# Optimization experiments

Hardware: AMD Instinct MI355X
Metric: run time of the kernel (lower is better)

## Reference

```python
import jax, jax.numpy as jnp
import numpy as np

NEG = -100000.0

def setup_inputs() -> dict:
    key = jax.random.key(0)
    k1, k2 = jax.random.split(key)
    B, La, Lb, D = 64, 512, 512, 768
    a = jax.random.normal(k1, (B, La, D), dtype=jnp.float32)
    b = jax.random.normal(k2, (B, Lb, D), dtype=jnp.float32)
    mask_a = jnp.ones((B, La), dtype=jnp.int32)
    mask_b = jnp.ones((B, Lb), dtype=jnp.int32)
    return {"a": a, "mask_a": mask_a, "b": b, "mask_b": mask_b}

def reference(a, mask_a, b, mask_b):
    # e: [B, La, Lb] raw alignment scores
    e = jnp.einsum('bid,bjd->bij', a, b)
    # outer-product mask [B, La, Lb]; masked_fill where mask_e < 0.5
    mask_e = mask_a[:, :, None].astype(jnp.float32) * mask_b[:, None, :].astype(jnp.float32)
    e = jnp.where(mask_e < 0.5, NEG, e)
    # softmax over Lb -> attend b for each position of a
    t_a = jnp.einsum('bij,bjd->bid', jax.nn.softmax(e, axis=2), b)
    # softmax over La -> attend a for each position of b (transpose of attn)
    t_b = jnp.einsum('bij,bid->bjd', jax.nn.softmax(e, axis=1), a)
    m_a = jnp.concatenate((a, t_a, a - t_a, a * t_a), axis=-1)
    m_b = jnp.concatenate((b, t_b, b - t_b, b * t_b), axis=-1)
    return (m_a, m_b)
```

## Files before the change

kernel.cpp:

```cpp
#include <hip/hip_runtime.h>
#include <stdint.h>

#define B_  64
#define LA  512
#define LB  512
#define DD  768
#define NEGV -100000.0f

typedef __attribute__((ext_vector_type(8))) short bf16x8;
typedef __attribute__((ext_vector_type(4))) float f32x4;

__device__ __forceinline__ unsigned short f2bf(float x) {
    union { float f; unsigned u; } v; v.f = x;
    unsigned r = v.u + 0x7fffu + ((v.u >> 16) & 1u);
    return (unsigned short)(r >> 16);
}
__device__ __forceinline__ float bf2f(unsigned short h) {
    union { float f; unsigned u; } v; v.u = ((unsigned)h) << 16;
    return v.f;
}

#define GLD16(gp, lp) __builtin_amdgcn_global_load_lds( \
    (const __attribute__((address_space(1))) void*)(gp), \
    (__attribute__((address_space(3))) void*)(lp), 16, 0, 0)

template<int L>
__global__ void prep_k(const float* __restrict__ x,
                       unsigned short* __restrict__ xT,
                       unsigned short* __restrict__ xh,
                       unsigned short* __restrict__ xl) {
    __shared__ unsigned short tile[64][65];
    const int l0 = blockIdx.x * 64, d0 = blockIdx.y * 64, b = blockIdx.z;
    const float* xp = x + (size_t)b * L * DD;
    unsigned short* tp = xT + (size_t)b * DD * L;
    unsigned short* hp = xh + (size_t)b * L * DD;
    unsigned short* lp = xl + (size_t)b * L * DD;
    const int c4 = (threadIdx.x & 15) * 4;
    const int r0 = threadIdx.x >> 4;
#pragma unroll
    for (int s = 0; s < 4; ++s) {
        const int r = r0 + s * 16;
        const int l = l0 + r;
        float4 v = *(const float4*)(xp + (size_t)l * DD + d0 + c4);
        ushort4 h, lo;
        h.x = f2bf(v.x); lo.x = f2bf(v.x - bf2f(h.x));
        h.y = f2bf(v.y); lo.y = f2bf(v.y - bf2f(h.y));
        h.z = f2bf(v.z); lo.z = f2bf(v.z - bf2f(h.z));
        h.w = f2bf(v.w); lo.w = f2bf(v.w - bf2f(h.w));
        tile[r][c4 + 0] = h.x; tile[r][c4 + 1] = h.y;
        tile[r][c4 + 2] = h.z; tile[r][c4 + 3] = h.w;
        const int qp = (((c4 >> 3) ^ (r >> 1)) & 3) << 3;
        const int dp = d0 + (c4 & ~31) + qp + (c4 & 7);
        *(ushort4*)&hp[(size_t)l * DD + dp] = h;
        *(ushort4*)&lp[(size_t)l * DD + dp] = lo;
    }
    __syncthreads();
    const int c = threadIdx.x & 63, rr = threadIdx.x >> 6;
#pragma unroll
    for (int s = 0; s < 16; ++s) {
        const int r = rr + s * 4;
        const int qp = (((c >> 3) ^ (r >> 1)) & 3) << 3;
        const int cp = l0 + (c & ~31) + qp + (c & 7);
        tp[(size_t)(d0 + r) * L + cp] = tile[c][r];
    }
}

__global__ __launch_bounds__(256, 2)
void egemm_k(const unsigned short* __restrict__ Ahg, const unsigned short* __restrict__ Alg,
             const unsigned short* __restrict__ Bhg, const unsigned short* __restrict__ Blg,
             const int* __restrict__ mask_a, const int* __restrict__ mask_b,
             float* __restrict__ e) {
    __shared__ unsigned short Ah[128 * 32], Al[128 * 32], Bh[128 * 32], Bl[128 * 32];
    const int loc = blockIdx.x, g = blockIdx.y;
    const int t = loc >> 3;
    const int bb = g * 8 + (loc & 7);
    const int m0 = (t & 3) * 128, n0 = (t >> 2) * 128;

    const int tid = threadIdx.x;
    const int lane = tid & 63, w = tid >> 6;
    const int wm = (w >> 1) * 64, wn = (w & 1) * 64;
    const int lrow = lane & 15, qsel = lane >> 4;
    const int poff = ((qsel ^ (lrow >> 1)) & 3) << 3;

    const size_t boff = (size_t)bb * 512 * DD;
    const int sr0 = (2 * w) * 16 + (lane >> 2);
    const int sc = (lane & 3) * 8;
    const unsigned short* pa0 = Ahg + boff + (size_t)(m0 + sr0) * DD + sc;
    const unsigned short* pa1 = pa0 + 16 * DD;
    const unsigned short* pl0 = Alg + boff + (size_t)(m0 + sr0) * DD + sc;
    const unsigned short* pl1 = pl0 + 16 * DD;
    const unsigned short* pb0 = Bhg + boff + (size_t)(n0 + sr0) * DD + sc;
    const unsigned short* pb1 = pb0 + 16 * DD;
    const unsigned short* pm0 = Blg + boff + (size_t)(n0 + sr0) * DD + sc;
    const unsigned short* pm1 = pm0 + 16 * DD;
    unsigned short* la0 = &Ah[(2 * w) * 512]; unsigned short* la1 = la0 + 512;
    unsigned short* ll0 = &Al[(2 * w) * 512]; unsigned short* ll1 = ll0 + 512;
    unsigned short* lb0 = &Bh[(2 * w) * 512]; unsigned short* lb1 = lb0 + 512;
    unsigned short* lm0 = &Bl[(2 * w) * 512]; unsigned short* lm1 = lm0 + 512;

    f32x4 acc[4][4] = {};

    for (int k0 = 0; k0 < DD; k0 += 32) {
        GLD16(pa0 + k0, la0); GLD16(pa1 + k0, la1);
        GLD16(pl0 + k0, ll0); GLD16(pl1 + k0, ll1);
        GLD16(pb0 + k0, lb0); GLD16(pb1 + k0, lb1);
        GLD16(pm0 + k0, lm0); GLD16(pm1 + k0, lm1);
        __syncthreads();
        bf16x8 ahf[4], alf[4], bhf[4], blf[4];
#pragma unroll
        for (int mi = 0; mi < 4; ++mi) {
            const int R = wm + mi * 16 + lrow;
            ahf[mi] = *(const bf16x8*)&Ah[R * 32 + poff];
            alf[mi] = *(const bf16x8*)&Al[R * 32 + poff];
        }
#pragma unroll
        for (int ni = 0; ni < 4; ++ni) {
            const int R = wn + ni * 16 + lrow;
            bhf[ni] = *(const bf16x8*)&Bh[R * 32 + poff];
            blf[ni] = *(const bf16x8*)&Bl[R * 32 + poff];
        }
#pragma unroll
        for (int mi = 0; mi < 4; ++mi)
#pragma unroll
            for (int ni = 0; ni < 4; ++ni) {
                acc[mi][ni] = __builtin_amdgcn_mfma_f32_16x16x32_bf16(alf[mi], bhf[ni], acc[mi][ni], 0, 0, 0);
                acc[mi][ni] = __builtin_amdgcn_mfma_f32_16x16x32_bf16(ahf[mi], blf[ni], acc[mi][ni], 0, 0, 0);
                acc[mi][ni] = __builtin_amdgcn_mfma_f32_16x16x32_bf16(ahf[mi], bhf[ni], acc[mi][ni], 0, 0, 0);
            }
        __syncthreads();
    }

    const int* map = mask_a + bb * LA;
    const int* mbp = mask_b + bb * LB;
    float* ep = e + (size_t)bb * LA * LB;
    const int colbase = n0 + wn + (lane & 15);
    const int rowbase = m0 + wm + (lane >> 4) * 4;
#pragma unroll
    for (int mi = 0; mi < 4; ++mi)
#pragma unroll
        for (int ni = 0; ni < 4; ++ni) {
            const int j = colbase + ni * 16;
            const float mbf = (float)mbp[j];
#pragma unroll
            for (int r = 0; r < 4; ++r) {
                const int i = rowbase + mi * 16 + r;
                const float mm = (float)map[i] * mbf;
                const float v = (mm < 0.5f) ? NEGV : acc[mi][ni][r];
                __builtin_nontemporal_store(v, &ep[(size_t)i * LB + j]);
            }
        }
}

__global__ void rowstats_k(const float* __restrict__ e,
                           float* __restrict__ rmax, float* __restrict__ rinv) {
    const int row = blockIdx.x * 4 + (threadIdx.x >> 6);
    const int lane = threadIdx.x & 63;
    const float* ep = e + (size_t)row * LB;
    float4 v1 = *(const float4*)(ep + lane * 8);
    float4 v2 = *(const float4*)(ep + lane * 8 + 4);
    float m = fmaxf(fmaxf(fmaxf(v1.x, v1.y), fmaxf(v1.z, v1.w)),
                    fmaxf(fmaxf(v2.x, v2.y), fmaxf(v2.z, v2.w)));
#pragma unroll
    for (int o = 32; o; o >>= 1) m = fmaxf(m, __shfl_xor(m, o));
    float s = __expf(v1.x - m) + __expf(v1.y - m) + __expf(v1.z - m) + __expf(v1.w - m)
            + __expf(v2.x - m) + __expf(v2.y - m) + __expf(v2.z - m) + __expf(v2.w - m);
#pragma unroll
    for (int o = 32; o; o >>= 1) s += __shfl_xor(s, o);
    if (lane == 0) { rmax[row] = m; rinv[row] = 1.0f / s; }
}

__global__ void colstats_k(const float* __restrict__ e,
                           float* __restrict__ cmax, float* __restrict__ cinv) {
    __shared__ float sm[4][64], ss[4][64];
    const int j0 = blockIdx.x * 64;
    const int bb = blockIdx.y;
    const int jj = threadIdx.x & 63, seg = threadIdx.x >> 6;
    const float* ep = e + (size_t)bb * LA * LB + (size_t)seg * 128 * LB + j0 + jj;
    float m = -3.4e38f, s = 0.f;
    for (int i = 0; i < 128; ++i) {
        const float v = ep[(size_t)i * LB];
        const float nm = fmaxf(m, v);
        s = s * __expf(m - nm) + __expf(v - nm);
        m = nm;
    }
    sm[seg][jj] = m; ss[seg][jj] = s;
    __syncthreads();
    if (seg == 0) {
        const float m0 = sm[0][jj], m1 = sm[1][jj], m2 = sm[2][jj], m3 = sm[3][jj];
        const float M = fmaxf(fmaxf(m0, m1), fmaxf(m2, m3));
        const float S = ss[0][jj] * __expf(m0 - M) + ss[1][jj] * __expf(m1 - M)
                      + ss[2][jj] * __expf(m2 - M) + ss[3][jj] * __expf(m3 - M);
        cmax[bb * LB + j0 + jj] = M;
        cinv[bb * LB + j0 + jj] = 1.0f / S;
    }
}

__global__ void pgen_k(const float* __restrict__ e,
                       const float* __restrict__ rmax, const float* __restrict__ rinv,
                       const float* __restrict__ cmax, const float* __restrict__ cinv,
                       unsigned short* __restrict__ Pa, unsigned short* __restrict__ PbT) {
    __shared__ unsigned short tile[64][65];
    const int i0 = blockIdx.x * 64, j0 = blockIdx.y * 64, bb = blockIdx.z;
    const float* ep = e + (size_t)bb * LA * LB;
    const int c = threadIdx.x & 63, r0 = threadIdx.x >> 6;
    const float cm = cmax[bb * LB + j0 + c];
    const float ci = cinv[bb * LB + j0 + c];
#pragma unroll
    for (int s = 0; s < 16; ++s) {
        const int r = r0 + s * 4;
        const float rm = rmax[bb * LA + i0 + r];
        const float ri = rinv[bb * LA + i0 + r];
        const float v = ep[(size_t)(i0 + r) * LB + j0 + c];
        const int qp = (((c >> 3) ^ (r >> 1)) & 3) << 3;
        const int jp = j0 + (c & ~31) + qp + (c & 7);
        Pa[((size_t)bb * LA + i0 + r) * LB + jp] = f2bf(__expf(v - rm) * ri);
        tile[r][c] = f2bf(__expf(v - cm) * ci);
    }
    __syncthreads();
#pragma unroll
    for (int s = 0; s < 16; ++s) {
        const int r = r0 + s * 4;
        const int qp = (((c >> 3) ^ (r >> 1)) & 3) << 3;
        const int ip = i0 + (c & ~31) + qp + (c & 7);
        PbT[((size_t)bb * LB + j0 + r) * LA + ip] = tile[c][r];
    }
}

__global__ __launch_bounds__(256, 2)
void pv_gemm_k(const unsigned short* __restrict__ P,
               const unsigned short* __restrict__ VT,
               const float* __restrict__ X,
               float* __restrict__ out) {
    constexpr int K = 512;
    __shared__ unsigned short At[128 * 32], Bt[128 * 32];
    const int loc = blockIdx.x, g = blockIdx.y;
    const int t = loc >> 3;
    const int bb = g * 8 + (loc & 7);
    const int m0 = (t & 3) * 128, n0 = (t >> 2) * 128;

    const int tid = threadIdx.x;
    const int lane = tid & 63, w = tid >> 6;
    const int wm = (w >> 1) * 64, wn = (w & 1) * 64;
    const int lrow = lane & 15, qsel = lane >> 4;
    const int poff = ((qsel ^ (lrow >> 1)) & 3) << 3;

    const unsigned short* Pp = P + (size_t)bb * 512 * K;
    const unsigned short* Vp = VT + (size_t)bb * DD * K;
    const int sr0 = (2 * w) * 16 + (lane >> 2);
    const int sc = (lane & 3) * 8;
    const unsigned short* p0 = Pp + (size_t)(m0 + sr0) * K + sc;
    const unsigned short* p1 = p0 + 16 * K;
    const unsigned short* v0 = Vp + (size_t)(n0 + sr0) * K + sc;
    const unsigned short* v1 = v0 + 16 * K;
    unsigned short* lA0 = &At[(2 * w) * 512]; unsigned short* lA1 = lA0 + 512;
    unsigned short* lB0 = &Bt[(2 * w) * 512]; unsigned short* lB1 = lB0 + 512;

    f32x4 acc[4][4] = {};
    for (int k0 = 0; k0 < K; k0 += 32) {
        GLD16(p0 + k0, lA0); GLD16(p1 + k0, lA1);
        GLD16(v0 + k0, lB0); GLD16(v1 + k0, lB1);
        __syncthreads();
        bf16x8 af[4], bf_[4];
#pragma unroll
        for (int mi = 0; mi < 4; ++mi)
            af[mi] = *(const bf16x8*)&At[(wm + mi * 16 + lrow) * 32 + poff];
#pragma unroll
        for (int ni = 0; ni < 4; ++ni)
            bf_[ni] = *(const bf16x8*)&Bt[(wn + ni * 16 + lrow) * 32 + poff];
#pragma unroll
        for (int mi = 0; mi < 4; ++mi)
#pragma unroll
            for (int ni = 0; ni < 4; ++ni)
                acc[mi][ni] = __builtin_amdgcn_mfma_f32_16x16x32_bf16(af[mi], bf_[ni], acc[mi][ni], 0, 0, 0);
        __syncthreads();
    }

    const float* Xp = X + (size_t)bb * 512 * DD;
    float* op = out + (size_t)bb * 512 * (4 * DD);
    const int colbase = n0 + wn + (lane & 15);
    const int rowbase = m0 + wm + (lane >> 4) * 4;
#pragma unroll
    for (int mi = 0; mi < 4; ++mi)
#pragma unroll
        for (int ni = 0; ni < 4; ++ni) {
            const int d = colbase + ni * 16;
#pragma unroll
            for (int r = 0; r < 4; ++r) {
                const int i = rowbase + mi * 16 + r;
                const float tv = acc[mi][ni][r];
                const float xv = Xp[(size_t)i * DD + d];
                float* o = op + (size_t)i * (4 * DD) + d;
                __builtin_nontemporal_store(xv, o);
                __builtin_nontemporal_store(tv, o + DD);
                __builtin_nontemporal_store(xv - tv, o + 2 * DD);
                __builtin_nontemporal_store(xv * tv, o + 3 * DD);
            }
        }
}

extern "C" void kernel_launch(void* const* d_in, const int* in_sizes, int n_in,
                              void* d_out, int out_size, void* d_ws, size_t ws_size,
                              hipStream_t stream) {
    const float* a      = (const float*)d_in[0];
    const int*   mask_a = (const int*)d_in[1];
    const float* b      = (const float*)d_in[2];
    const int*   mask_b = (const int*)d_in[3];
    float* out = (float*)d_out;

    uint8_t* w = (uint8_t*)d_ws;
    float* e            = (float*)w;          w += (size_t)B_ * LA * LB * 4;
    unsigned short* aT  = (unsigned short*)w; w += (size_t)B_ * DD * LA * 2;
    unsigned short* bT  = (unsigned short*)w; w += (size_t)B_ * DD * LB * 2;
    unsigned short* ahi = (unsigned short*)w; w += (size_t)B_ * LA * DD * 2;
    unsigned short* alo = (unsigned short*)w; w += (size_t)B_ * LA * DD * 2;
    unsigned short* bhi = (unsigned short*)w; w += (size_t)B_ * LB * DD * 2;
    unsigned short* blo = (unsigned short*)w; w += (size_t)B_ * LB * DD * 2;
    float* rmax = (float*)w; w += (size_t)B_ * LA * 4;
    float* rinv = (float*)w; w += (size_t)B_ * LA * 4;
    float* cmax = (float*)w; w += (size_t)B_ * LB * 4;
    float* cinv = (float*)w; w += (size_t)B_ * LB * 4;
    unsigned short* Pa  = ahi;
    unsigned short* PbT = ahi + (size_t)B_ * LA * LB;

    prep_k<LA><<<dim3(LA / 64, DD / 64, B_), 256, 0, stream>>>(a, aT, ahi, alo);
    prep_k<LB><<<dim3(LB / 64, DD / 64, B_), 256, 0, stream>>>(b, bT, bhi, blo);
    egemm_k<<<dim3(128, 8), 256, 0, stream>>>(ahi, alo, bhi, blo, mask_a, mask_b, e);
    rowstats_k<<<B_ * LA / 4, 256, 0, stream>>>(e, rmax, rinv);
    colstats_k<<<dim3(LB / 64, B_), 256, 0, stream>>>(e, cmax, cinv);
    pgen_k<<<dim3(LA / 64, LB / 64, B_), 256, 0, stream>>>(e, rmax, rinv, cmax, cinv, Pa, PbT);
    float* out_mb = out + (size_t)B_ * LA * (4 * DD);
    pv_gemm_k<<<dim3(192, 8), 256, 0, stream>>>(Pa, bT, a, out);
    pv_gemm_k<<<dim3(192, 8), 256, 0, stream>>>(PbT, aT, b, out_mb);
}
```

Baseline: 1.362 ms.

## Fuse all stages into one persistent kernel with software grid barriers

Replaces the eight separate launches (prep, score GEMM, row/col stats, probability generation, two PV GEMMs) with one persistent kernel of 512 blocks that loops over work items per phase and synchronises phases with an atomic grid barrier. This removes launch gaps and tail effects between stages and lets the two PV GEMMs share one work pool. Pa/PbT get dedicated workspace instead of aliasing ahi, and the nontemporal store on e is dropped. It risks deadlock if all 512 blocks are not co-resident, and the barriers serialise phases with fixed grid-wide parallelism, which may underuse the GPU in some phases.

```diff
diff --git a/kernel.cpp b/kernel.cpp
--- a/kernel.cpp
+++ b/kernel.cpp
@@ -6,6 +6,7 @@
 #define LB  512
 #define DD  768
 #define NEGV -100000.0f
+#define NB  512
 
 typedef __attribute__((ext_vector_type(8))) short bf16x8;
 typedef __attribute__((ext_vector_type(4))) float f32x4;
@@ -24,278 +25,314 @@
     (const __attribute__((address_space(1))) void*)(gp), \
     (__attribute__((address_space(3))) void*)(lp), 16, 0, 0)
 
-template<int L>
-__global__ void prep_k(const float* __restrict__ x,
-                       unsigned short* __restrict__ xT,
-                       unsigned short* __restrict__ xh,
-                       unsigned short* __restrict__ xl) {
-    __shared__ unsigned short tile[64][65];
-    const int l0 = blockIdx.x * 64, d0 = blockIdx.y * 64, b = blockIdx.z;
-    const float* xp = x + (size_t)b * L * DD;
-    unsigned short* tp = xT + (size_t)b * DD * L;
-    unsigned short* hp = xh + (size_t)b * L * DD;
-    unsigned short* lp = xl + (size_t)b * L * DD;
-    const int c4 = (threadIdx.x & 15) * 4;
-    const int r0 = threadIdx.x >> 4;
-#pragma unroll
-    for (int s = 0; s < 4; ++s) {
-        const int r = r0 + s * 16;
-        const int l = l0 + r;
-        float4 v = *(const float4*)(xp + (size_t)l * DD + d0 + c4);
-        ushort4 h, lo;
-        h.x = f2bf(v.x); lo.x = f2bf(v.x - bf2f(h.x));
-        h.y = f2bf(v.y); lo.y = f2bf(v.y - bf2f(h.y));
-        h.z = f2bf(v.z); lo.z = f2bf(v.z - bf2f(h.z));
-        h.w = f2bf(v.w); lo.w = f2bf(v.w - bf2f(h.w));
-        tile[r][c4 + 0] = h.x; tile[r][c4 + 1] = h.y;
-        tile[r][c4 + 2] = h.z; tile[r][c4 + 3] = h.w;
-        const int qp = (((c4 >> 3) ^ (r >> 1)) & 3) << 3;
-        const int dp = d0 + (c4 & ~31) + qp + (c4 & 7);
-        *(ushort4*)&hp[(size_t)l * DD + dp] = h;
-        *(ushort4*)&lp[(size_t)l * DD + dp] = lo;
-    }
+__device__ __forceinline__ void gridbar(unsigned* cnt, unsigned* gen) {
     __syncthreads();
-    const int c = threadIdx.x & 63, rr = threadIdx.x >> 6;
-#pragma unroll
-    for (int s = 0; s < 16; ++s) {
-        const int r = rr + s * 4;
-        const int qp = (((c >> 3) ^ (r >> 1)) & 3) << 3;
-        const int cp = l0 + (c & ~31) + qp + (c & 7);
-        tp[(size_t)(d0 + r) * L + cp] = tile[c][r];
-    }
+    if (threadIdx.x == 0) {
+        __threadfence();
+        unsigned g0 = __hip_atomic_load(gen, __ATOMIC_ACQUIRE, __HIP_MEMORY_SCOPE_AGENT);
+        unsigned t = __hip_atomic_fetch_add(cnt, 1u, __ATOMIC_ACQ_REL, __HIP_MEMORY_SCOPE_AGENT);
+        if (t == NB - 1) {
+            __hip_atomic_store(cnt, 0u, __ATOMIC_RELAXED, __HIP_MEMORY_SCOPE_AGENT);
+            __hip_atomic_fetch_add(gen, 1u, __ATOMIC_ACQ_REL, __HIP_MEMORY_SCOPE_AGENT);
+        } else {
+            while (__hip_atomic_load(gen, __ATOMIC_ACQUIRE, __HIP_MEMORY_SCOPE_AGENT) == g0)
+                __builtin_amdgcn_s_sleep(8);
+        }
+        __threadfence();
+    }
+    __syncthreads();
+}
+
+__global__ void init_sync_k(unsigned* cnt, unsigned* gen) {
+    if (threadIdx.x == 0) { *cnt = 0u; *gen = 0u; }
 }
 
 __global__ __launch_bounds__(256, 2)
-void egemm_k(const unsigned short* __restrict__ Ahg, const unsigned short* __restrict__ Alg,
-             const unsigned short* __restrict__ Bhg, const unsigned short* __restrict__ Blg,
-             const int* __restrict__ mask_a, const int* __restrict__ mask_b,
-             float* __restrict__ e) {
-    __shared__ unsigned short Ah[128 * 32], Al[128 * 32], Bh[128 * 32], Bl[128 * 32];
-    const int loc = blockIdx.x, g = blockIdx.y;
-    const int t = loc >> 3;
-    const int bb = g * 8 + (loc & 7);
-    const int m0 = (t & 3) * 128, n0 = (t >> 2) * 128;
-
+void mega_k(const float* __restrict__ a, const float* __restrict__ b,
+            const int* __restrict__ mask_a, const int* __restrict__ mask_b,
+            float* __restrict__ e,
+            unsigned short* __restrict__ aT, unsigned short* __restrict__ bT,
+            unsigned short* __restrict__ ahi, unsigned short* __restrict__ alo,
+            unsigned short* __restrict__ bhi, unsigned short* __restrict__ blo,
+            float* __restrict__ rmax, float* __restrict__ rinv,
+            float* __restrict__ cmax, float* __restrict__ cinv,
+            unsigned short* __restrict__ Pa, unsigned short* __restrict__ PbT,
+            float* __restrict__ out_a, float* __restrict__ out_b,
+            unsigned* cnt, unsigned* gen)
+{
+    __shared__ __align__(16) unsigned char SMEM[32768];
+    const int bid = blockIdx.x;
     const int tid = threadIdx.x;
-    const int lane = tid & 63, w = tid >> 6;
-    const int wm = (w >> 1) * 64, wn = (w & 1) * 64;
-    const int lrow = lane & 15, qsel = lane >> 4;
-    const int poff = ((qsel ^ (lrow >> 1)) & 3) << 3;
-
-    const size_t boff = (size_t)bb * 512 * DD;
-    const int sr0 = (2 * w) * 16 + (lane >> 2);
-    const int sc = (lane & 3) * 8;
-    const unsigned short* pa0 = Ahg + boff + (size_t)(m0 + sr0) * DD + sc;
-    const unsigned short* pa1 = pa0 + 16 * DD;
-    const unsigned short* pl0 = Alg + boff + (size_t)(m0 + sr0) * DD + sc;
-    const unsigned short* pl1 = pl0 + 16 * DD;
-    const unsigned short* pb0 = Bhg + boff + (size_t)(n0 + sr0) * DD + sc;
-    const unsigned short* pb1 = pb0 + 16 * DD;
-    const unsigned short* pm0 = Blg + boff + (size_t)(n0 + sr0) * DD + sc;
-    const unsigned short* pm1 = pm0 + 16 * DD;
-    unsigned short* la0 = &Ah[(2 * w) * 512]; unsigned short* la1 = la0 + 512;
-    unsigned short* ll0 = &Al[(2 * w) * 512]; unsigned short* ll1 = ll0 + 512;
-    unsigned short* lb0 = &Bh[(2 * w) * 512]; unsigned short* lb1 = lb0 + 512;
-    unsigned short* lm0 = &Bl[(2 * w) * 512]; unsigned short* lm1 = lm0 + 512;
-
-    f32x4 acc[4][4] = {};
-
-    for (int k0 = 0; k0 < DD; k0 += 32) {
-        GLD16(pa0 + k0, la0); GLD16(pa1 + k0, la1);
-        GLD16(pl0 + k0, ll0); GLD16(pl1 + k0, ll1);
-        GLD16(pb0 + k0, lb0); GLD16(pb1 + k0, lb1);
-        GLD16(pm0 + k0, lm0); GLD16(pm1 + k0, lm1);
+
+    {
+        unsigned short (*tile)[65] = reinterpret_cast<unsigned short(*)[65]>(SMEM);
+        const int c4 = (tid & 15) * 4;
+        const int r0 = tid >> 4;
+        const int c = tid & 63, rr = tid >> 6;
+        for (int job = bid; job < 12288; job += NB) {
+            __syncthreads();
+            const int side = (job >= 6144);
+            const int j = side ? job - 6144 : job;
+            const int x = j & 7, y = (j >> 3) % 12, bb = j / 96;
+            const int l0 = x * 64, d0 = y * 64;
+            const float* xp = (side ? b : a) + (size_t)bb * 512 * DD;
+            unsigned short* tp = (side ? bT : aT) + (size_t)bb * DD * 512;
+            unsigned short* hp = (side ? bhi : ahi) + (size_t)bb * 512 * DD;
+            unsigned short* lp = (side ? blo : alo) + (size_t)bb * 512 * DD;
+#pragma unroll
+            for (int s = 0; s < 4; ++s) {
+                const int r = r0 + s * 16;
+                const int l = l0 + r;
+                float4 v = *(const float4*)(xp + (size_t)l * DD + d0 + c4);
+                ushort4 h, lo;
+                h.x = f2bf(v.x); lo.x = f2bf(v.x - bf2f(h.x));
+                h.y = f2bf(v.y); lo.y = f2bf(v.y - bf2f(h.y));
+                h.z = f2bf(v.z); lo.z = f2bf(v.z - bf2f(h.z));
+                h.w = f2bf(v.w); lo.w = f2bf(v.w - bf2f(h.w));
+                tile[r][c4 + 0] = h.x; tile[r][c4 + 1] = h.y;
+                tile[r][c4 + 2] = h.z; tile[r][c4 + 3] = h.w;
+                const int qp = (((c4 >> 3) ^ (r >> 1)) & 3) << 3;
+                const int dp = d0 + (c4 & ~31) + qp + (c4 & 7);
+                *(ushort4*)&hp[(size_t)l * DD + dp] = h;
+                *(ushort4*)&lp[(size_t)l * DD + dp] = lo;
+            }
+            __syncthreads();
+#pragma unroll
+            for (int s = 0; s < 16; ++s) {
+                const int r = rr + s * 4;
+                const int qp = (((c >> 3) ^ (r >> 1)) & 3) << 3;
+                const int cp = l0 + (c & ~31) + qp + (c & 7);
+                tp[(size_t)(d0 + r) * 512 + cp] = tile[c][r];
+            }
+        }
+    }
+    gridbar(cnt, gen);
+
+    {
+        unsigned short* Ah = (unsigned short*)SMEM;
+        unsigned short* Al = Ah + 4096;
+        unsigned short* Bh = Ah + 8192;
+        unsigned short* Bl = Ah + 12288;
+        const int lane = tid & 63, w = tid >> 6;
+        const int wm = (w >> 1) * 64, wn = (w & 1) * 64;
+        const int lrow = lane & 15, qsel = lane >> 4;
+        const int poff = ((qsel ^ (lrow >> 1)) & 3) << 3;
+        const int sr0 = (2 * w) * 16 + (lane >> 2);
+        const int sc = (lane & 3) * 8;
+        unsigned short* la0 = &Ah[(2 * w) * 512]; unsigned short* la1 = la0 + 512;
+        unsigned short* ll0 = &Al[(2 * w) * 512]; unsigned short* ll1 = ll0 + 512;
+        unsigned short* lb0 = &Bh[(2 * w) * 512]; unsigned short* lb1 = lb0 + 512;
+        unsigned short* lm0 = &Bl[(2 * w) * 512]; unsigned short* lm1 = lm0 + 512;
+
+        for (int job = bid; job < 1024; job += NB) {
+            const int bb = job >> 4, t = job & 15;
+            const int m0 = (t & 3) * 128, n0 = (t >> 2) * 128;
+            const size_t boff = (size_t)bb * 512 * DD;
+            const unsigned short* pa0 = ahi + boff + (size_t)(m0 + sr0) * DD + sc;
+            const unsigned short* pa1 = pa0 + 16 * DD;
+            const unsigned short* pl0 = alo + boff + (size_t)(m0 + sr0) * DD + sc;
+            const unsigned short* pl1 = pl0 + 16 * DD;
+            const unsigned short* pb0 = bhi + boff + (size_t)(n0 + sr0) * DD + sc;
+            const unsigned short* pb1 = pb0 + 16 * DD;
+            const unsigned short* pm0 = blo + boff + (size_t)(n0 + sr0) * DD + sc;
+            const unsigned short* pm1 = pm0 + 16 * DD;
+
+            f32x4 acc[4][4] = {};
+            for (int k0 = 0; k0 < DD; k0 += 32) {
+                GLD16(pa0 + k0, la0); GLD16(pa1 + k0, la1);
+                GLD16(pl0 + k0, ll0); GLD16(pl1 + k0, ll1);
+                GLD16(pb0 + k0, lb0); GLD16(pb1 + k0, lb1);
+                GLD16(pm0 + k0, lm0); GLD16(pm1 + k0, lm1);
+                __syncthreads();
+                bf16x8 ahf[4], alf[4], bhf[4], blf[4];
+#pragma unroll
+                for (int mi = 0; mi < 4; ++mi) {
+                    const int R = wm + mi * 16 + lrow;
+                    ahf[mi] = *(const bf16x8*)&Ah[R * 32 + poff];
+                    alf[mi] = *(const bf16x8*)&Al[R * 32 + poff];
+                }
+#pragma unroll
+                for (int ni = 0; ni < 4; ++ni) {
+                    const int R = wn + ni * 16 + lrow;
+                    bhf[ni] = *(const bf16x8*)&Bh[R * 32 + poff];
+                    blf[ni] = *(const bf16x8*)&Bl[R * 32 + poff];
+                }
+#pragma unroll
+                for (int mi = 0; mi < 4; ++mi)
+#pragma unroll
+                    for (int ni = 0; ni < 4; ++ni) {
+                        acc[mi][ni] = __builtin_amdgcn_mfma_f32_16x16x32_bf16(alf[mi], bhf[ni], acc[mi][ni], 0, 0, 0);
+                        acc[mi][ni] = __builtin_amdgcn_mfma_f32_16x16x32_bf16(ahf[mi], blf[ni], acc[mi][ni], 0, 0, 0);
+                        acc[mi][ni] = __builtin_amdgcn_mfma_f32_16x16x32_bf16(ahf[mi], bhf[ni], acc[mi][ni], 0, 0, 0);
+                    }
+                __syncthreads();
+            }
+
+            const int* map = mask_a + bb * LA;
+            const int* mbp = mask_b + bb * LB;
+            float* ep = e + (size_t)bb * LA * LB;
+            const int colbase = n0 + wn + (lane & 15);
+            const int rowbase = m0 + wm + (lane >> 4) * 4;
+#pragma unroll
+            for (int mi = 0; mi < 4; ++mi)
+#pragma unroll
+                for (int ni = 0; ni < 4; ++ni) {
+                    const int jx = colbase + ni * 16;
+                    const float mbf = (float)mbp[jx];
+#pragma unroll
+                    for (int r = 0; r < 4; ++r) {
+                        const int ix = rowbase + mi * 16 + r;
+                        const float mm = (float)map[ix] * mbf;
+                        ep[(size_t)ix * LB + jx] = (mm < 0.5f) ? NEGV : acc[mi][ni][r];
+                    }
+                }
+        }
+    }
+    gridbar(cnt, gen);
+
+    {
+        float* sm = (float*)SMEM;
+        float* ss = sm + 256;
+        const int jj = tid & 63, seg = tid >> 6;
+        const int j0 = (bid & 7) * 64, bb = bid >> 3;
+        const float* ep = e + (size_t)bb * LA * LB + (size_t)seg * 128 * LB + j0 + jj;
+        float m = -3.4e38f, s = 0.f;
+        for (int i = 0; i < 128; ++i) {
+            const float v = ep[(size_t)i * LB];
+            const float nm = fmaxf(m, v);
+            s = s * __expf(m - nm) + __expf(v - nm);
+            m = nm;
+        }
+        sm[seg * 64 + jj] = m; ss[seg * 64 + jj] = s;
         __syncthreads();
-        bf16x8 ahf[4], alf[4], bhf[4], blf[4];
-#pragma unroll
-        for (int mi = 0; mi < 4; ++mi) {
-            const int R = wm + mi * 16 + lrow;
-            ahf[mi] = *(const bf16x8*)&Ah[R * 32 + poff];
-            alf[mi] = *(const bf16x8*)&Al[R * 32 + poff];
-        }
-#pragma unroll
-        for (int ni = 0; ni < 4; ++ni) {
-            const int R = wn + ni * 16 + lrow;
-            bhf[ni] = *(const bf16x8*)&Bh[R * 32 + poff];
-            blf[ni] = *(const bf16x8*)&Bl[R * 32 + poff];
-        }
-#pragma unroll
-        for (int mi = 0; mi < 4; ++mi)
-#pragma unroll
-            for (int ni = 0; ni < 4; ++ni) {
-                acc[mi][ni] = __builtin_amdgcn_mfma_f32_16x16x32_bf16(alf[mi], bhf[ni], acc[mi][ni], 0, 0, 0);
-                acc[mi][ni] = __builtin_amdgcn_mfma_f32_16x16x32_bf16(ahf[mi], blf[ni], acc[mi][ni], 0, 0, 0);
-                acc[mi][ni] = __builtin_amdgcn_mfma_f32_16x16x32_bf16(ahf[mi], bhf[ni], acc[mi][ni], 0, 0, 0);
-            }
-        __syncthreads();
-    }
-
-    const int* map = mask_a + bb * LA;
-    const int* mbp = mask_b + bb * LB;
-    float* ep = e + (size_t)bb * LA * LB;
-    const int colbase = n0 + wn + (lane & 15);
-    const int rowbase = m0 + wm + (lane >> 4) * 4;
-#pragma unroll
-    for (int mi = 0; mi < 4; ++mi)
-#pragma unroll
-        for (int ni = 0; ni < 4; ++ni) {
-            const int j = colbase + ni * 16;
-            const float mbf = (float)mbp[j];
-#pragma unroll
-            for (int r = 0; r < 4; ++r) {
-                const int i = rowbase + mi * 16 + r;
-                const float mm = (float)map[i] * mbf;
-                const float v = (mm < 0.5f) ? NEGV : acc[mi][ni][r];
-                __builtin_nontemporal_store(v, &ep[(size_t)i * LB + j]);
-            }
-        }
-}
-
-__global__ void rowstats_k(const float* __restrict__ e,
-                           float* __restrict__ rmax, float* __restrict__ rinv) {
-    const int row = blockIdx.x * 4 + (threadIdx.x >> 6);
-    const int lane = threadIdx.x & 63;
-    const float* ep = e + (size_t)row * LB;
-    float4 v1 = *(const float4*)(ep + lane * 8);
-    float4 v2 = *(const float4*)(ep + lane * 8 + 4);
-    float m = fmaxf(fmaxf(fmaxf(v1.x, v1.y), fmaxf(v1.z, v1.w)),
-                    fmaxf(fmaxf(v2.x, v2.y), fmaxf(v2.z, v2.w)));
-#pragma unroll
-    for (int o = 32; o; o >>= 1) m = fmaxf(m, __shfl_xor(m, o));
-    float s = __expf(v1.x - m) + __expf(v1.y - m) + __expf(v1.z - m) + __expf(v1.w - m)
-            + __expf(v2.x - m) + __expf(v2.y - m) + __expf(v2.z - m) + __expf(v2.w - m);
-#pragma unroll
-    for (int o = 32; o; o >>= 1) s += __shfl_xor(s, o);
-    if (lane == 0) { rmax[row] = m; rinv[row] = 1.0f / s; }
-}
-
-__global__ void colstats_k(const float* __restrict__ e,
-                           float* __restrict__ cmax, float* __restrict__ cinv) {
-    __shared__ float sm[4][64], ss[4][64];
-    const int j0 = blockIdx.x * 64;
-    const int bb = blockIdx.y;
-    const int jj = threadIdx.x & 63, seg = threadIdx.x >> 6;
-    const float* ep = e + (size_t)bb * LA * LB + (size_t)seg * 128 * LB + j0 + jj;
-    float m = -3.4e38f, s = 0.f;
-    for (int i = 0; i < 128; ++i) {
-        const float v = ep[(size_t)i * LB];
-        const float nm = fmaxf(m, v);
-        s = s * __expf(m - nm) + __expf(v - nm);
-        m = nm;
-    }
-    sm[seg][jj] = m; ss[seg][jj] = s;
-    __syncthreads();
-    if (seg == 0) {
-        const float m0 = sm[0][jj], m1 = sm[1][jj], m2 = sm[2][jj], m3 = sm[3][jj];
-        const float M = fmaxf(fmaxf(m0, m1), fmaxf(m2, m3));
-        const float S = ss[0][jj] * __expf(m0 - M) + ss[1][jj] * __expf(m1 - M)
-                      + ss[2][jj] * __expf(m2 - M) + ss[3][jj] * __expf(m3 - M);
-        cmax[bb * LB + j0 + jj] = M;
-        cinv[bb * LB + j0 + jj] = 1.0f / S;
-    }
-}
-
-__global__ void pgen_k(const float* __restrict__ e,
-                       const float* __restrict__ rmax, const float* __restrict__ rinv,
-                       const float* __restrict__ cmax, const float* __restrict__ cinv,
-                       unsigned short* __restrict__ Pa, unsigned short* __restrict__ PbT) {
-    __shared__ unsigned short tile[64][65];
-    const int i0 = blockIdx.x * 64, j0 = blockIdx.y * 64, bb = blockIdx.z;
-    const float* ep = e + (size_t)bb * LA * LB;
-    const int c = threadIdx.x & 63, r0 = threadIdx.x >> 6;
-    const float cm = cmax[bb * LB + j0 + c];
-    const float ci = cinv[bb * LB + j0 + c];
-#pragma unroll
-    for (int s = 0; s < 16; ++s) {
-        const int r = r0 + s * 4;
-        const float rm = rmax[bb * LA + i0 + r];
-        const float ri = rinv[bb * LA + i0 + r];
-        const float v = ep[(size_t)(i0 + r) * LB + j0 + c];
-        const int qp = (((c >> 3) ^ (r >> 1)) & 3) << 3;
-        const int jp = j0 + (c & ~31) + qp + (c & 7);
-        Pa[((size_t)bb * LA + i0 + r) * LB + jp] = f2bf(__expf(v - rm) * ri);
-        tile[r][c] = f2bf(__expf(v - cm) * ci);
-    }
-    __syncthreads();
-#pragma unroll
-    for (int s = 0; s < 16; ++s) {
-        const int r = r0 + s * 4;
-        const int qp = (((c >> 3) ^ (r >> 1)) & 3) << 3;
-        const int ip = i0 + (c & ~31) + qp + (c & 7);
-        PbT[((size_t)bb * LB + j0 + r) * LA + ip] = tile[c][r];
-    }
-}
-
-__global__ __launch_bounds__(256, 2)
-void pv_gemm_k(const unsigned short* __restrict__ P,
-               const unsigned short* __restrict__ VT,
-               const float* __restrict__ X,
-               float* __restrict__ out) {
-    constexpr int K = 512;
-    __shared__ unsigned short At[128 * 32], Bt[128 * 32];
-    const int loc = blockIdx.x, g = blockIdx.y;
-    const int t = loc >> 3;
-    const int bb = g * 8 + (loc & 7);
-    const int m0 = (t & 3) * 128, n0 = (t >> 2) * 128;
-
-    const int tid = threadIdx.x;
-    const int lane = tid & 63, w = tid >> 6;
-    const int wm = (w >> 1) * 64, wn = (w & 1) * 64;
-    const int lrow = lane & 15, qsel = lane >> 4;
-    const int poff = ((qsel ^ (lrow >> 1)) & 3) << 3;
-
-    const unsigned short* Pp = P + (size_t)bb * 512 * K;
-    const unsigned short* Vp = VT + (size_t)bb * DD * K;
-    const int sr0 = (2 * w) * 16 + (lane >> 2);
-    const int sc = (lane & 3) * 8;
-    const unsigned short* p0 = Pp + (size_t)(m0 + sr0) * K + sc;
-    const unsigned short* p1 = p0 + 16 * K;
-    const unsigned short* v0 = Vp + (size_t)(n0 + sr0) * K + sc;
-    const unsigned short* v1 = v0 + 16 * K;
-    unsigned short* lA0 = &At[(2 * w) * 512]; unsigned short* lA1 = lA0 + 512;
-    unsigned short* lB0 = &Bt[(2 * w) * 512]; unsigned short* lB1 = lB0 + 512;
-
-    f32x4 acc[4][4] = {};
-    for (int k0 = 0; k0 < K; k0 += 32) {
-        GLD16(p0 + k0, lA0); GLD16(p1 + k0, lA1);
-        GLD16(v0 + k0, lB0); GLD16(v1 + k0, lB1);
-        __syncthreads();
-        bf16x8 af[4], bf_[4];
-#pragma unroll
-        for (int mi = 0; mi < 4; ++mi)
-            af[mi] = *(const bf16x8*)&At[(wm + mi * 16 + lrow) * 32 + poff];
-#pragma unroll
-        for (int ni = 0; ni < 4; ++ni)
-            bf_[ni] = *(const bf16x8*)&Bt[(wn + ni * 16 + lrow) * 32 + poff];
-#pragma unroll
-        for (int mi = 0; mi < 4; ++mi)
-#pragma unroll
-            for (int ni = 0; ni < 4; ++ni)
-                acc[mi][ni] = __builtin_amdgcn_mfma_f32_16x16x32_bf16(af[mi], bf_[ni], acc[mi][ni], 0, 0, 0);
-        __syncthreads();
-    }
-
-    const float* Xp = X + (size_t)bb * 512 * DD;
-    float* op = out + (size_t)bb * 512 * (4 * DD);
-    const int colbase = n0 + wn + (lane & 15);
-    const int rowbase = m0 + wm + (lane >> 4) * 4;
-#pragma unroll
-    for (int mi = 0; mi < 4; ++mi)
-#pragma unroll
-        for (int ni = 0; ni < 4; ++ni) {
-            const int d = colbase + ni * 16;
-#pragma unroll
-            for (int r = 0; r < 4; ++r) {
-                const int i = rowbase + mi * 16 + r;
-                const float tv = acc[mi][ni][r];
-                const float xv = Xp[(size_t)i * DD + d];
-                float* o = op + (size_t)i * (4 * DD) + d;
-                __builtin_nontemporal_store(xv, o);
-                __builtin_nontemporal_store(tv, o + DD);
-                __builtin_nontemporal_store(xv - tv, o + 2 * DD);
-                __builtin_nontemporal_store(xv * tv, o + 3 * DD);
-            }
-        }
+        if (seg == 0) {
+            const float m0 = sm[jj], m1 = sm[64 + jj], m2 = sm[128 + jj], m3 = sm[192 + jj];
+            const float M = fmaxf(fmaxf(m0, m1), fmaxf(m2, m3));
+            const float S = ss[jj] * __expf(m0 - M) + ss[64 + jj] * __expf(m1 - M)
+                          + ss[128 + jj] * __expf(m2 - M) + ss[192 + jj] * __expf(m3 - M);
+            cmax[bb * LB + j0 + jj] = M;
+            cinv[bb * LB + j0 + jj] = 1.0f / S;
+        }
+        const int lane = tid & 63;
+        for (int q = 0; q < 16; ++q) {
+            const int row = (bid + q * NB) * 4 + (tid >> 6);
+            const float* rp = e + (size_t)row * LB;
+            float4 v1 = *(const float4*)(rp + lane * 8);
+            float4 v2 = *(const float4*)(rp + lane * 8 + 4);
+            float rm = fmaxf(fmaxf(fmaxf(v1.x, v1.y), fmaxf(v1.z, v1.w)),
+                             fmaxf(fmaxf(v2.x, v2.y), fmaxf(v2.z, v2.w)));
+#pragma unroll
+            for (int o = 32; o; o >>= 1) rm = fmaxf(rm, __shfl_xor(rm, o));
+            float rs = __expf(v1.x - rm) + __expf(v1.y - rm) + __expf(v1.z - rm) + __expf(v1.w - rm)
+                     + __expf(v2.x - rm) + __expf(v2.y - rm) + __expf(v2.z - rm) + __expf(v2.w - rm);
+#pragma unroll
+            for (int o = 32; o; o >>= 1) rs += __shfl_xor(rs, o);
+            if (lane == 0) { rmax[row] = rm; rinv[row] = 1.0f / rs; }
+        }
+    }
+    gridbar(cnt, gen);
+
+    {
+        unsigned short (*tile)[65] = reinterpret_cast<unsigned short(*)[65]>(SMEM);
+        const int c = tid & 63, r0 = tid >> 6;
+        for (int job = bid; job < 4096; job += NB) {
+            __syncthreads();
+            const int i0 = (job & 7) * 64, j0 = ((job >> 3) & 7) * 64, bb = job >> 6;
+            const float* ep = e + (size_t)bb * LA * LB;
+            const float cm = cmax[bb * LB + j0 + c];
+            const float ci = cinv[bb * LB + j0 + c];
+#pragma unroll
+            for (int s = 0; s < 16; ++s) {
+                const int r = r0 + s * 4;
+                const float rm = rmax[bb * LA + i0 + r];
+                const float ri = rinv[bb * LA + i0 + r];
+                const float v = ep[(size_t)(i0 + r) * LB + j0 + c];
+                const int qp = (((c >> 3) ^ (r >> 1)) & 3) << 3;
+                const int jp = j0 + (c & ~31) + qp + (c & 7);
+                Pa[((size_t)bb * LA + i0 + r) * LB + jp] = f2bf(__expf(v - rm) * ri);
+                tile[r][c] = f2bf(__expf(v - cm) * ci);
+            }
+            __syncthreads();
+#pragma unroll
+            for (int s = 0; s < 16; ++s) {
+                const int r = r0 + s * 4;
+                const int qp = (((c >> 3) ^ (r >> 1)) & 3) << 3;
+                const int ip = i0 + (c & ~31) + qp + (c & 7);
+                PbT[((size_t)bb * LB + j0 + r) * LA + ip] = tile[c][r];
+            }
+        }
+    }
+    gridbar(cnt, gen);
+
+    {
+        unsigned short* At = (unsigned short*)SMEM;
+        unsigned short* Bt = At + 4096;
+        const int lane = tid & 63, w = tid >> 6;
+        const int wm = (w >> 1) * 64, wn = (w & 1) * 64;
+        const int lrow = lane & 15, qsel = lane >> 4;
+        const int poff = ((qsel ^ (lrow >> 1)) & 3) << 3;
+        const int sr0 = (2 * w) * 16 + (lane >> 2);
+        const int sc = (lane & 3) * 8;
+        unsigned short* lA0 = &At[(2 * w) * 512]; unsigned short* lA1 = lA0 + 512;
+        unsigned short* lB0 = &Bt[(2 * w) * 512]; unsigned short* lB1 = lB0 + 512;
+
+        for (int job = bid; job < 3072; job += NB) {
+            const int side = (job >= 1536);
+            const int jj = side ? job - 1536 : job;
+            const int bb = jj / 24;
+            const int t = jj - bb * 24;
+            const int m0 = (t & 3) * 128, n0 = (t >> 2) * 128;
+            const unsigned short* Pp = (side ? PbT : Pa) + (size_t)bb * 512 * 512;
+            const unsigned short* Vp = (side ? aT : bT) + (size_t)bb * DD * 512;
+            const float* Xp = (side ? b : a) + (size_t)bb * 512 * DD;
+            float* op = (side ? out_b : out_a) + (size_t)bb * 512 * (4 * DD);
+
+            const unsigned short* p0 = Pp + (size_t)(m0 + sr0) * 512 + sc;
+            const unsigned short* p1 = p0 + 16 * 512;
+            const unsigned short* v0 = Vp + (size_t)(n0 + sr0) * 512 + sc;
+            const unsigned short* v1 = v0 + 16 * 512;
+
+            f32x4 acc[4][4] = {};
+            for (int k0 = 0; k0 < 512; k0 += 32) {
+                GLD16(p0 + k0, lA0); GLD16(p1 + k0, lA1);
+                GLD16(v0 + k0, lB0); GLD16(v1 + k0, lB1);
+                __syncthreads();
+                bf16x8 af[4], bf_[4];
+#pragma unroll
+                for (int mi = 0; mi < 4; ++mi)
+                    af[mi] = *(const bf16x8*)&At[(wm + mi * 16 + lrow) * 32 + poff];
+#pragma unroll
+                for (int ni = 0; ni < 4; ++ni)
+                    bf_[ni] = *(const bf16x8*)&Bt[(wn + ni * 16 + lrow) * 32 + poff];
+#pragma unroll
+                for (int mi = 0; mi < 4; ++mi)
+#pragma unroll
+                    for (int ni = 0; ni < 4; ++ni)
+                        acc[mi][ni] = __builtin_amdgcn_mfma_f32_16x16x32_bf16(af[mi], bf_[ni], acc[mi][ni], 0, 0, 0);
+                __syncthreads();
+            }
+
+            const int colbase = n0 + wn + (lane & 15);
+            const int rowbase = m0 + wm + (lane >> 4) * 4;
+#pragma unroll
+            for (int mi = 0; mi < 4; ++mi)
+#pragma unroll
+                for (int ni = 0; ni < 4; ++ni) {
+                    const int d = colbase + ni * 16;
+#pragma unroll
+                    for (int r = 0; r < 4; ++r) {
+                        const int ix = rowbase + mi * 16 + r;
+                        const float tv = acc[mi][ni][r];
+                        const float xv = Xp[(size_t)ix * DD + d];
+                        float* o = op + (size_t)ix * (4 * DD) + d;
+                        __builtin_nontemporal_store(xv, o);
+                        __builtin_nontemporal_store(tv, o + DD);
+                        __builtin_nontemporal_store(xv - tv, o + 2 * DD);
+                        __builtin_nontemporal_store(xv * tv, o + 3 * DD);
+                    }
+                }
+        }
+    }
 }
 
 extern "C" void kernel_launch(void* const* d_in, const int* in_sizes, int n_in,
@@ -315,20 +352,21 @@
     unsigned short* alo = (unsigned short*)w; w += (size_t)B_ * LA * DD * 2;
     unsigned short* bhi = (unsigned short*)w; w += (size_t)B_ * LB * DD * 2;
     unsigned short* blo = (unsigned short*)w; w += (size_t)B_ * LB * DD * 2;
+    unsigned short* Pa  = (unsigned short*)w; w += (size_t)B_ * LA * LB * 2;
+    unsigned short* PbT = (unsigned short*)w; w += (size_t)B_ * LB * LA * 2;
     float* rmax = (float*)w; w += (size_t)B_ * LA * 4;
     float* rinv = (float*)w; w += (size_t)B_ * LA * 4;
     float* cmax = (float*)w; w += (size_t)B_ * LB * 4;
     float* cinv = (float*)w; w += (size_t)B_ * LB * 4;
-    unsigned short* Pa  = ahi;
-    unsigned short* PbT = ahi + (size_t)B_ * LA * LB;
-
-    prep_k<LA><<<dim3(LA / 64, DD / 64, B_), 256, 0, stream>>>(a, aT, ahi, alo);
-    prep_k<LB><<<dim3(LB / 64, DD / 64, B_), 256, 0, stream>>>(b, bT, bhi, blo);
-    egemm_k<<<dim3(128, 8), 256, 0, stream>>>(ahi, alo, bhi, blo, mask_a, mask_b, e);
-    rowstats_k<<<B_ * LA / 4, 256, 0, stream>>>(e, rmax, rinv);
-    colstats_k<<<dim3(LB / 64, B_), 256, 0, stream>>>(e, cmax, cinv);
-    pgen_k<<<dim3(LA / 64, LB / 64, B_), 256, 0, stream>>>(e, rmax, rinv, cmax, cinv, Pa, PbT);
-    float* out_mb = out + (size_t)B_ * LA * (4 * DD);
-    pv_gemm_k<<<dim3(192, 8), 256, 0, stream>>>(Pa, bT, a, out);
-    pv_gemm_k<<<dim3(192, 8), 256, 0, stream>>>(PbT, aT, b, out_mb);
-}
+    unsigned* cnt = (unsigned*)w; w += 64;
+    unsigned* gen = (unsigned*)w; w += 64;
+
+    float* out_a = out;
+    float* out_b = out + (size_t)B_ * LA * (4 * DD);
+
+    init_sync_k<<<1, 64, 0, stream>>>(cnt, gen);
+    mega_k<<<NB, 256, 0, stream>>>(a, b, mask_a, mask_b, e,
+                                   aT, bT, ahi, alo, bhi, blo,
+                                   rmax, rinv, cmax, cinv, Pa, PbT,
+                                   out_a, out_b, cnt, gen);
+}
```

Measured after the change: 1.771 ms. 1.3x slower.
